# Kernel optimization log

Hardware: AMD Instinct MI355X
Metric: run time of the kernel (lower is better)

The kernel has to match this reference:

```python
import jax, jax.numpy as jnp
import numpy as np

B, S, HID, NH = 2, 2048, 2048, 16
HD = HID // NH          # head_size = 128
ROPE_THETA = 10000.0
SCALING = HD ** -0.5


def setup_inputs() -> dict:
    key = jax.random.key(0)
    ks = jax.random.split(key, 8)
    std = 1.0 / np.sqrt(HID)
    inp = {
        "hidden_states": jax.random.normal(ks[0], (B, S, HID), jnp.float32),
        "positions": jnp.broadcast_to(jnp.arange(S, dtype=jnp.int32), (B, S)),
        "wq": jax.random.normal(ks[1], (HID, HID), jnp.float32) * std,
        "bq": jax.random.normal(ks[2], (HID,), jnp.float32) * 0.02,
        "wk": jax.random.normal(ks[3], (HID, HID), jnp.float32) * std,
        "bk": jax.random.normal(ks[4], (HID,), jnp.float32) * 0.02,
        "wv": jax.random.normal(ks[5], (HID, HID), jnp.float32) * std,
        "bv": jax.random.normal(ks[6], (HID,), jnp.float32) * 0.02,
        "wc": jax.random.normal(ks[7], (HID, HID), jnp.float32) * std,
    }
    return inp


def _rope_neox(x, positions):
    # x: [B, S, NH, HD]; positions: [B, S] int
    half = HD // 2
    inv_freq = 1.0 / (ROPE_THETA ** (jnp.arange(half, dtype=jnp.float32) * (2.0 / HD)))
    freqs = positions.astype(jnp.float32)[..., None] * inv_freq      # [B,S,half]
    cos = jnp.cos(freqs)[:, :, None, :]                               # [B,S,1,half]
    sin = jnp.sin(freqs)[:, :, None, :]
    x1, x2 = x[..., :half], x[..., half:]
    return jnp.concatenate([x1 * cos - x2 * sin, x2 * cos + x1 * sin], axis=-1)


def reference(hidden_states, positions, wq, bq, wk, bk, wv, bv, wc):
    # fused QKV projections
    q = hidden_states @ wq + bq
    k = hidden_states @ wk + bk
    v = hidden_states @ wv + bv
    q = q.reshape(B, S, NH, HD)
    k = k.reshape(B, S, NH, HD)
    v = v.reshape(B, S, NH, HD)
    # neox-style rotary embedding over full head dim
    q = _rope_neox(q, positions)
    k = _rope_neox(k, positions)
    # causal self-attention (prefill path of RadixAttention)
    scores = jnp.einsum("bqhd,bkhd->bhqk", q, k) * SCALING
    causal = jnp.tril(jnp.ones((S, S), dtype=bool))
    scores = jnp.where(causal, scores, jnp.finfo(scores.dtype).min)
    probs = jax.nn.softmax(scores, axis=-1)
    attn = jnp.einsum("bhqk,bkhd->bqhd", probs, v).reshape(B, S, HID)
    # output projection (no bias)
    return attn @ wc
```

## Files before the change

kernel.cpp:

```cpp
#include <hip/hip_runtime.h>
#include <stdint.h>

constexpr int Bsz = 2;
constexpr int Ssz = 2048;
constexpr int Hid = 2048;
constexpr int NHd = 16;
constexpr int Hd  = 128;
constexpr int Mrows = Bsz * Ssz;

typedef __bf16 bf16;
typedef __bf16 bf16x8 __attribute__((ext_vector_type(8)));
typedef __bf16 bf16x4 __attribute__((ext_vector_type(4)));
typedef float  f32x4  __attribute__((ext_vector_type(4)));
typedef float  f32x16 __attribute__((ext_vector_type(16)));

__device__ __forceinline__ void gload_lds16(const bf16* g, bf16* l) {
  __builtin_amdgcn_global_load_lds((const __attribute__((address_space(1))) void*)g,
                                   (__attribute__((address_space(3))) void*)l, 16, 0, 0);
}

__device__ __forceinline__ uint32_t pkbf(bf16 a, bf16 b) {
  union { bf16 hh[2]; uint32_t u; } x;
  x.hh[0] = a; x.hh[1] = b;
  return x.u;
}
__device__ __forceinline__ uint32_t pkff(float a, float b) {
  return pkbf((bf16)a, (bf16)b);
}

__global__ void k_cvt(const float* __restrict__ in, bf16* __restrict__ out, int n4) {
  int i = blockIdx.x * blockDim.x + threadIdx.x;
  if (i >= n4) return;
  float4 v = ((const float4*)in)[i];
  bf16x4 o = { (bf16)v.x, (bf16)v.y, (bf16)v.z, (bf16)v.w };
  ((bf16x4*)out)[i] = o;
}

__global__ void k_wtrans(const float* __restrict__ w0, const float* __restrict__ w1,
                         const float* __restrict__ w2, const float* __restrict__ w3,
                         bf16* __restrict__ out) {
  __shared__ float tile[64][65];
  const int z = blockIdx.z;
  const float* w = (z == 0) ? w0 : (z == 1) ? w1 : (z == 2) ? w2 : w3;
  bf16* o = out + (size_t)z * Hid * Hid;
  const int n0 = blockIdx.x * 64, k0 = blockIdx.y * 64;
  const int tid = threadIdx.x;
  {
    const int row = tid >> 4, col = (tid & 15) * 4;
#pragma unroll
    for (int i = 0; i < 4; i++) {
      float4 v = *(const float4*)&w[(size_t)(k0 + row + i * 16) * Hid + n0 + col];
      tile[row + i * 16][col + 0] = v.x;
      tile[row + i * 16][col + 1] = v.y;
      tile[row + i * 16][col + 2] = v.z;
      tile[row + i * 16][col + 3] = v.w;
    }
  }
  __syncthreads();
  {
    const int n = tid >> 2, ks = (tid & 3) * 16;
    union { bf16x8 v[2]; bf16 e[16]; } pk;
#pragma unroll
    for (int j = 0; j < 16; j++) pk.e[j] = (bf16)tile[ks + j][n];
    bf16* op = &o[(size_t)(n0 + n) * Hid + k0 + ks];
    *(bf16x8*)op = pk.v[0];
    *(bf16x8*)(op + 8) = pk.v[1];
  }
}

__device__ __forceinline__ bf16x8 rdfrag(const bf16* t, int row, int kslot) {
  return *(const bf16x8*)((const char*)t + row * 128 + (((kslot ^ (row & 7)) & 7) << 4));
}

__device__ __forceinline__ void stage_half(const bf16* g, bf16* l, int w, int lane) {
  const int rsub = lane >> 3;
  const int slot = (lane & 7) ^ rsub;
#pragma unroll
  for (int j = 0; j < 2; ++j) {
    const int blk = w * 2 + j;
    gload_lds16(g + (size_t)(blk * 8 + rsub) * Hid + slot * 8, l + blk * 512);
  }
}

__device__ __forceinline__ void stage_192(const bf16* g, bf16* l, int w, int lane) {
  const int rsub = lane >> 3;
  const int slot = (lane & 7) ^ rsub;
#pragma unroll
  for (int j = 0; j < 3; ++j) {
    const int blk = w * 3 + j;
    gload_lds16(g + (size_t)(blk * 8 + rsub) * Hid + slot * 8, l + blk * 512);
  }
}

#define PH_BAR() __builtin_amdgcn_s_barrier()

__global__ __launch_bounds__(512, 1) void k_qkv(const bf16* __restrict__ A,
                                                const bf16* __restrict__ Bt,
                                                const float* __restrict__ biasq,
                                                const float* __restrict__ biask,
                                                const float* __restrict__ biasv,
                                                bf16* __restrict__ Qo, bf16* __restrict__ Ko,
                                                bf16* __restrict__ Vo) {
  constexpr int KK = Hid;
  constexpr int NT = KK / 64;
  __shared__ bf16 smA[2][256 * 64];
  __shared__ bf16 smB[3][192 * 64];
  const int hw = blockIdx.y * gridDim.x + blockIdx.x;
  const int chunk = hw & 7, within = hw >> 3;
  const int cr = chunk & 1, cc = chunk >> 1;
  const int mt = cr * 8 + (within & 7);
  const int nt = cc * 8 + (within >> 3);
  const int m0 = mt * 256, n0 = nt * 192;
  const int tid = threadIdx.x, lane = tid & 63, w = tid >> 6;
  const int wm = w >> 2, wn = w & 3;
  const int frow = lane & 15, a4 = lane >> 4;
  const bf16* Ag = A + (size_t)m0 * KK;
  const bf16* Bg = Bt + (size_t)n0 * KK;
  f32x4 acc[8][3] = {};
  stage_half(Ag,                    smA[0],            w, lane);
  stage_half(Ag + (size_t)128 * KK, smA[0] + 128 * 64, w, lane);
  stage_192 (Bg,                    smB[0],            w, lane);
  stage_192 (Bg + 64,               smB[1],            w, lane);
  asm volatile("s_waitcnt vmcnt(3)" ::: "memory");
  __builtin_amdgcn_sched_barrier(0);
  __builtin_amdgcn_s_barrier();
  for (int kt = 0; kt < NT; ++kt) {
    const bf16* At  = smA[kt & 1];
    const bf16* Btl = smB[kt % 3];
    const bool more1 = (kt + 1) < NT;
    const bool more2 = (kt + 2) < NT;
    bf16x8 afA[4][2], afB[4][2], bfr[3][2];
#pragma unroll
    for (int f = 0; f < 4; ++f)
#pragma unroll
      for (int kk = 0; kk < 2; ++kk)
        afA[f][kk] = rdfrag(At, wm * 128 + f * 16 + frow, kk * 4 + a4);
#pragma unroll
    for (int nf = 0; nf < 3; ++nf)
#pragma unroll
      for (int kk = 0; kk < 2; ++kk)
        bfr[nf][kk] = rdfrag(Btl, wn * 48 + nf * 16 + frow, kk * 4 + a4);
    if (more1) {
      bf16* As2 = smA[(kt + 1) & 1];
      const size_t kn = (size_t)(kt + 1) * 64;
      stage_half(Ag + kn,                    As2,            w, lane);
      stage_half(Ag + (size_t)128 * KK + kn, As2 + 128 * 64, w, lane);
    }
    PH_BAR();
    __builtin_amdgcn_s_setprio(1);
#pragma unroll
    for (int f = 0; f < 4; ++f)
#pragma unroll
      for (int nf = 0; nf < 2; ++nf)
#pragma unroll
        for (int kk = 0; kk < 2; ++kk)
          acc[f][nf] = __builtin_amdgcn_mfma_f32_16x16x32_bf16(
              afA[f][kk], bfr[nf][kk], acc[f][nf], 0, 0, 0);
    __builtin_amdgcn_s_setprio(0);
    __builtin_amdgcn_s_barrier();
#pragma unroll
    for (int f = 0; f < 4; ++f)
#pragma unroll
      for (int kk = 0; kk < 2; ++kk)
        afB[f][kk] = rdfrag(At, wm * 128 + 64 + f * 16 + frow, kk * 4 + a4);
    if (more2) stage_192(Bg + (size_t)(kt + 2) * 64, smB[(kt + 2) % 3], w, lane);
    PH_BAR();
    __builtin_amdgcn_s_setprio(1);
#pragma unroll
    for (int f = 0; f < 4; ++f)
#pragma unroll
      for (int nf = 0; nf < 2; ++nf)
#pragma unroll
        for (int kk = 0; kk < 2; ++kk)
          acc[4 + f][nf] = __builtin_amdgcn_mfma_f32_16x16x32_bf16(
              afB[f][kk], bfr[nf][kk], acc[4 + f][nf], 0, 0, 0);
    __builtin_amdgcn_s_setprio(0);
    __builtin_amdgcn_s_barrier();
    __builtin_amdgcn_s_setprio(1);
#pragma unroll
    for (int f = 0; f < 4; ++f)
#pragma unroll
      for (int kk = 0; kk < 2; ++kk)
        acc[f][2] = __builtin_amdgcn_mfma_f32_16x16x32_bf16(
            afA[f][kk], bfr[2][kk], acc[f][2], 0, 0, 0);
#pragma unroll
    for (int f = 0; f < 4; ++f)
#pragma unroll
      for (int kk = 0; kk < 2; ++kk)
        acc[4 + f][2] = __builtin_amdgcn_mfma_f32_16x16x32_bf16(
            afB[f][kk], bfr[2][kk], acc[4 + f][2], 0, 0, 0);
    __builtin_amdgcn_s_setprio(0);
    if (more1) {
      if (more2) { asm volatile("s_waitcnt vmcnt(3)" ::: "memory"); }
      else       { asm volatile("s_waitcnt vmcnt(0)" ::: "memory"); }
      __builtin_amdgcn_sched_barrier(0);
    }
    __builtin_amdgcn_s_barrier();
  }
#pragma unroll
  for (int nf = 0; nf < 3; ++nf) {
    const int col = n0 + wn * 48 + nf * 16 + frow;
    const int z = col >> 11;
    const float* bias = (z == 0) ? biasq : (z == 1) ? biask : biasv;
    bf16* o = (z == 0) ? Qo : (z == 1) ? Ko : Vo;
    const float oscale = (z == 1) ? (float)(0.08838834764831845 * 1.4426950408889634) : 1.0f;
    const float bb_ = bias[col & 2047];
    const int h = (col >> 7) & 15, hd = col & (Hd - 1);
#pragma unroll
    for (int mf = 0; mf < 8; ++mf) {
#pragma unroll
      for (int r = 0; r < 4; ++r) {
        const int row = m0 + wm * 128 + mf * 16 + a4 * 4 + r;
        const int bb = row >> 11, ss = row & (Ssz - 1);
        o[(((size_t)bb * NHd + h) * Ssz + ss) * Hd + hd] = (bf16)((acc[mf][nf][r] + bb_) * oscale);
      }
    }
  }
}

template <int CHM, int CHN>
__global__ __launch_bounds__(512, 1) void k_gemm(const bf16* __restrict__ A,
                                                 const bf16* __restrict__ Bt,
                                                 float* __restrict__ Fo) {
  constexpr int KK = Hid;
  constexpr int NT = KK / 64;
  __shared__ bf16 smA[2][256 * 64];
  __shared__ bf16 smB[3][128 * 64];
  const int hw = blockIdx.y * gridDim.x + blockIdx.x;
  const int chunk = hw & 7, within = hw >> 3;
  const int chunk_rows = gridDim.y / CHM;
  const int cr = chunk % chunk_rows, cc = chunk / chunk_rows;
  const int mt = cr * CHM + within % CHM;
  const int nt = cc * CHN + within / CHM;
  const int m0 = mt * 256, n0 = nt * 128;
  const int tid = threadIdx.x, lane = tid & 63, w = tid >> 6;
  const int wm = w >> 2, wn = w & 3;
  const int frow = lane & 15, a4 = lane >> 4;
  const bf16* Ag = A + (size_t)m0 * KK;
  const bf16* Bg = Bt + (size_t)n0 * KK;
  f32x4 acc[8][2] = {};
  stage_half(Ag,                    smA[0],            w, lane);
  stage_half(Ag + (size_t)128 * KK, smA[0] + 128 * 64, w, lane);
  stage_half(Bg,                    smB[0],            w, lane);
  stage_half(Bg + 64,               smB[1],            w, lane);
  asm volatile("s_waitcnt vmcnt(2)" ::: "memory");
  __builtin_amdgcn_sched_barrier(0);
  __builtin_amdgcn_s_barrier();
  for (int kt = 0; kt < NT; ++kt) {
    const bf16* At  = smA[kt & 1];
    const bf16* Btl = smB[kt % 3];
    const bool more1 = (kt + 1) < NT;
    const bool more2 = (kt + 2) < NT;
    bf16x8 afA[4][2], afB[4][2], bfr[2][2];
#pragma unroll
    for (int f = 0; f < 4; ++f)
#pragma unroll
      for (int kk = 0; kk < 2; ++kk)
        afA[f][kk] = rdfrag(At, wm * 128 + f * 16 + frow, kk * 4 + a4);
#pragma unroll
    for (int nf = 0; nf < 2; ++nf)
#pragma unroll
      for (int kk = 0; kk < 2; ++kk)
        bfr[nf][kk] = rdfrag(Btl, wn * 32 + nf * 16 + frow, kk * 4 + a4);
    if (more1) {
      bf16* As2 = smA[(kt + 1) & 1];
      const size_t kn = (size_t)(kt + 1) * 64;
      stage_half(Ag + kn,                    As2,            w, lane);
      stage_half(Ag + (size_t)128 * KK + kn, As2 + 128 * 64, w, lane);
    }
    PH_BAR();
    __builtin_amdgcn_s_setprio(1);
#pragma unroll
    for (int f = 0; f < 4; ++f)
#pragma unroll
      for (int nf = 0; nf < 2; ++nf)
#pragma unroll
        for (int kk = 0; kk < 2; ++kk)
          acc[f][nf] = __builtin_amdgcn_mfma_f32_16x16x32_bf16(
              afA[f][kk], bfr[nf][kk], acc[f][nf], 0, 0, 0);
    __builtin_amdgcn_s_setprio(0);
    __builtin_amdgcn_s_barrier();
#pragma unroll
    for (int f = 0; f < 4; ++f)
#pragma unroll
      for (int kk = 0; kk < 2; ++kk)
        afB[f][kk] = rdfrag(At, wm * 128 + 64 + f * 16 + frow, kk * 4 + a4);
    if (more2) stage_half(Bg + (size_t)(kt + 2) * 64, smB[(kt + 2) % 3], w, lane);
    PH_BAR();
    __builtin_amdgcn_s_setprio(1);
#pragma unroll
    for (int f = 0; f < 4; ++f)
#pragma unroll
      for (int nf = 0; nf < 2; ++nf)
#pragma unroll
        for (int kk = 0; kk < 2; ++kk)
          acc[4 + f][nf] = __builtin_amdgcn_mfma_f32_16x16x32_bf16(
              afB[f][kk], bfr[nf][kk], acc[4 + f][nf], 0, 0, 0);
    __builtin_amdgcn_s_setprio(0);
    if (more1) {
      if (more2) { asm volatile("s_waitcnt vmcnt(2)" ::: "memory"); }
      else       { asm volatile("s_waitcnt vmcnt(0)" ::: "memory"); }
      __builtin_amdgcn_sched_barrier(0);
    }
    __builtin_amdgcn_s_barrier();
  }
#pragma unroll
  for (int mf = 0; mf < 8; ++mf)
#pragma unroll
    for (int nf = 0; nf < 2; ++nf) {
      const int col = n0 + wn * 32 + nf * 16 + frow;
#pragma unroll
      for (int r = 0; r < 4; ++r) {
        const int row = m0 + wm * 128 + mf * 16 + a4 * 4 + r;
        Fo[(size_t)row * Hid + col] = acc[mf][nf][r];
      }
    }
}

__global__ void k_rope(bf16* __restrict__ Kk, const int* __restrict__ pos) {
  const int idx = blockIdx.x * 256 + threadIdx.x;
  const int i = idx & 63;
  const int s = (idx >> 6) & (Ssz - 1);
  const int bh = idx >> 17;
  const int b = bh >> 4;
  const float p = (float)pos[b * Ssz + s];
  const float f = p * exp2f(-(float)i * 0.20762050593046014f);
  float sn, cs;
  sincosf(f, &sn, &cs);
  const size_t base = ((size_t)bh * Ssz + s) * Hd;
  float x1 = (float)Kk[base + i], x2 = (float)Kk[base + i + 64];
  Kk[base + i]      = (bf16)(x1 * cs - x2 * sn);
  Kk[base + i + 64] = (bf16)(x2 * cs + x1 * sn);
}

__global__ __launch_bounds__(256, 2) void k_attn(const bf16* __restrict__ Qg,
                                                 const bf16* __restrict__ Kg,
                                                 const bf16* __restrict__ Vg,
                                                 const int* __restrict__ pos,
                                                 bf16* __restrict__ AO) {
  const int bid = blockIdx.x;
  const int slot = bid & 255;
  const int bh = slot & 31;
  const int xch = slot >> 5;
  const int qc = (bid >> 8) ? (15 - xch) : xch;
  const int tid = threadIdx.x, lane = tid & 63, w = tid >> 6;
  const int l31 = lane & 31, h = lane >> 5;
  __shared__ bf16 Ks[2][64 * 128];
  __shared__ bf16 Vt[2][128 * 72];
  const size_t hbase = (size_t)bh * Ssz * Hd;
  const int q0 = qc * 128 + w * 32;
  bf16x8 qf[8];
  {
    const bf16* qp = Qg + hbase + (size_t)(q0 + l31) * Hd + h * 8;
#pragma unroll
    for (int c = 0; c < 8; c++) qf[c] = *(const bf16x8*)(qp + c * 16);
  }
  {
    const float p = (float)pos[(bh >> 4) * Ssz + (q0 + l31)];
#pragma unroll
    for (int c = 0; c < 4; c++) {
#pragma unroll
      for (int j = 0; j < 8; j++) {
        const int i = c * 16 + 8 * h + j;
        const float f = p * exp2f(-(float)i * 0.20762050593046014f);
        float sn, cs;
        sincosf(f, &sn, &cs);
        const float x1 = (float)qf[c][j], x2 = (float)qf[c + 4][j];
        qf[c][j]     = (bf16)(x1 * cs - x2 * sn);
        qf[c + 4][j] = (bf16)(x2 * cs + x1 * sn);
      }
    }
  }
  float m = -1e30f, lsum = 0.f;
  f32x16 o[4] = {};
  const int NT = 2 * (qc + 1);
  const int r4  = (tid >> 4) << 2;
  const int hd0 = (tid & 15) << 3;
  bf16x8 vv[4];
#pragma unroll
  for (int p = 0; p < 4; p++)
    vv[p] = *(const bf16x8*)(Vg + hbase + (size_t)(r4 + p) * Hd + hd0);
  __builtin_amdgcn_sched_barrier(0);
#pragma unroll
  for (int i = 0; i < 4; i++) {
    const int db  = (w * 4 + i) * 1024 + (lane << 4);
    const int row = db >> 8;
    const int cb  = (db & 255) ^ ((row & 7) << 4);
    gload_lds16(Kg + hbase + row * Hd + (cb >> 1), Ks[0] + (w * 4 + i) * 512);
  }
  for (int t = 0; t < NT; ++t) {
    const int kv0 = t * 64;
    const int cur = t & 1;
    asm volatile("s_waitcnt vmcnt(4)" ::: "memory");
#pragma unroll
    for (int j = 0; j < 8; j++) {
      uint2 wv;
      wv.x = pkbf(vv[0][j], vv[1][j]);
      wv.y = pkbf(vv[2][j], vv[3][j]);
      const int hd = hd0 + j;
      const int cb = (r4 * 2) ^ (((hd >> 3) & 7) << 4);
      *(uint2*)((char*)(Vt[cur]) + hd * 144 + cb) = wv;
    }
    const int tn = (t + 1 < NT) ? t + 1 : t;
    const size_t nb = (size_t)tn * 64;
#pragma unroll
    for (int p = 0; p < 4; p++)
      vv[p] = *(const bf16x8*)(Vg + hbase + (nb + r4 + p) * Hd + hd0);
    __builtin_amdgcn_sched_barrier(0);
#pragma unroll
    for (int i = 0; i < 4; i++) {
      const int db  = (w * 4 + i) * 1024 + (lane << 4);
      const int row = db >> 8;
      const int cb  = (db & 255) ^ ((row & 7) << 4);
      gload_lds16(Kg + hbase + (nb + row) * Hd + (cb >> 1), Ks[cur ^ 1] + (w * 4 + i) * 512);
    }
    asm volatile("s_waitcnt vmcnt(8) lgkmcnt(0)" ::: "memory");
    __builtin_amdgcn_sched_barrier(0);
    __builtin_amdgcn_s_barrier();
    if (kv0 <= q0 + 31) {
      const bf16* KsC = Ks[cur];
      const bf16* VtC = Vt[cur];
      f32x16 s0 = {}, s1 = {};
      __builtin_amdgcn_s_setprio(1);
#pragma unroll
      for (int c = 0; c < 8; c++) {
        const int cb = (c * 32 + h * 16) ^ ((l31 & 7) << 4);
        bf16x8 k0 = *(const bf16x8*)((const char*)KsC + l31 * 256 + cb);
        bf16x8 k1 = *(const bf16x8*)((const char*)KsC + (32 + l31) * 256 + cb);
        s0 = __builtin_amdgcn_mfma_f32_32x32x16_bf16(k0, qf[c], s0, 0, 0, 0);
        s1 = __builtin_amdgcn_mfma_f32_32x32x16_bf16(k1, qf[c], s1, 0, 0, 0);
      }
      __builtin_amdgcn_s_setprio(0);
      if (kv0 + 63 > q0) {
        const int qg = q0 + l31;
        const int kb = kv0 + 4 * h;
#pragma unroll
        for (int r = 0; r < 16; r++) {
          const int cr = (r & 3) + 8 * (r >> 2);
          if (kb + cr > qg)      s0[r] = -1e30f;
          if (kb + 32 + cr > qg) s1[r] = -1e30f;
        }
      }
      float tm = s0[0];
#pragma unroll
      for (int r = 1; r < 16; r++) tm = fmaxf(tm, s0[r]);
#pragma unroll
      for (int r = 0; r < 16; r++) tm = fmaxf(tm, s1[r]);
      tm = fmaxf(tm, __shfl_xor(tm, 32));
      if (!__all(tm - m <= 8.0f)) {
        const float mn = fmaxf(m, tm);
        const float rs = exp2f(m - mn);
        m = mn; lsum *= rs;
#pragma unroll
        for (int ct = 0; ct < 4; ct++)
#pragma unroll
          for (int r = 0; r < 16; r++) o[ct][r] *= rs;
      }
      float ps = 0.f;
#pragma unroll
      for (int r = 0; r < 16; r++) { s0[r] = exp2f(s0[r] - m); ps += s0[r]; }
#pragma unroll
      for (int r = 0; r < 16; r++) { s1[r] = exp2f(s1[r] - m); ps += s1[r]; }
      ps += __shfl_xor(ps, 32);
      lsum += ps;
      uint32_t gw[8][2];
#pragma unroll
      for (int g = 0; g < 4; g++) {
        gw[g][0]     = pkff(s0[4 * g], s0[4 * g + 1]);
        gw[g][1]     = pkff(s0[4 * g + 2], s0[4 * g + 3]);
        gw[4 + g][0] = pkff(s1[4 * g], s1[4 * g + 1]);
        gw[4 + g][1] = pkff(s1[4 * g + 2], s1[4 * g + 3]);
      }
#pragma unroll
      for (int kc = 0; kc < 4; kc++) {
        const uint32_t a0 = gw[2 * kc][0], a1 = gw[2 * kc][1];
        const uint32_t b0 = gw[2 * kc + 1][0], b1 = gw[2 * kc + 1][1];
        const uint32_t sd0 = h ? a0 : b0, sd1 = h ? a1 : b1;
        const uint32_t r0 = (uint32_t)__shfl_xor((int)sd0, 32);
        const uint32_t r1 = (uint32_t)__shfl_xor((int)sd1, 32);
        union { uint32_t u[4]; bf16x8 v; } pa;
        pa.u[0] = h ? r0 : a0; pa.u[1] = h ? r1 : a1;
        pa.u[2] = h ? b0 : r0; pa.u[3] = h ? b1 : r1;
        __builtin_amdgcn_s_setprio(1);
#pragma unroll
        for (int ct = 0; ct < 4; ct++) {
          const int row = ct * 32 + l31;
          const int cb = (kc * 32 + h * 16) ^ (((row >> 3) & 7) << 4);
          bf16x8 vf = *(const bf16x8*)((const char*)VtC + row * 144 + cb);
          o[ct] = __builtin_amdgcn_mfma_f32_32x32x16_bf16(pa.v, vf, o[ct], 0, 0, 0);
        }
        __builtin_amdgcn_s_setprio(0);
      }
    }
    __builtin_amdgcn_s_barrier();
  }
  const float linv = 1.0f / lsum;
  float li[16];
#pragma unroll
  for (int r = 0; r < 16; r++)
    li[r] = __shfl(linv, (r & 3) + 8 * (r >> 2) + 4 * h);
  const int b = bh >> 4, hh = bh & 15;
#pragma unroll
  for (int ct = 0; ct < 4; ct++) {
#pragma unroll
    for (int r = 0; r < 16; r++) {
      const int qrow = q0 + (r & 3) + 8 * (r >> 2) + 4 * h;
      AO[((size_t)b * Ssz + qrow) * Hid + hh * Hd + ct * 32 + l31] = (bf16)(o[ct][r] * li[r]);
    }
  }
}

extern "C" void kernel_launch(void* const* d_in, const int* in_sizes, int n_in,
                              void* d_out, int out_size, void* d_ws, size_t ws_size,
                              hipStream_t stream) {
  (void)in_sizes; (void)n_in; (void)out_size; (void)ws_size;
  const float* hidden   = (const float*)d_in[0];
  const int*   positions= (const int*)d_in[1];
  const float* wq = (const float*)d_in[2];
  const float* bq = (const float*)d_in[3];
  const float* wk = (const float*)d_in[4];
  const float* bk = (const float*)d_in[5];
  const float* wv = (const float*)d_in[6];
  const float* bv = (const float*)d_in[7];
  const float* wc = (const float*)d_in[8];
  float* out = (float*)d_out;

  char* ws = (char*)d_ws;
  bf16* WT  = (bf16*)ws;
  bf16* Hbf = (bf16*)(ws + (size_t)4 * Hid * Hid * 2);
  bf16* Qb  = (bf16*)(ws + (size_t)4 * Hid * Hid * 2 + (size_t)Mrows * Hid * 2);
  bf16* Kb  = Qb + (size_t)Mrows * Hid;
  bf16* Vb  = Kb + (size_t)Mrows * Hid;

  k_cvt<<<dim3(Mrows * Hid / 4 / 256), dim3(256), 0, stream>>>(hidden, Hbf, Mrows * Hid / 4);
  k_wtrans<<<dim3(Hid / 64, Hid / 64, 4), dim3(256), 0, stream>>>(wq, wk, wv, wc, WT);
  k_qkv<<<dim3(32, 16), dim3(512), 0, stream>>>(
      Hbf, WT, bq, bk, bv, Qb, Kb, Vb);
  k_rope<<<dim3(Bsz * NHd * Ssz * 64 / 256), dim3(256), 0, stream>>>(Kb, positions);
  k_attn<<<dim3(512), dim3(256), 0, stream>>>(Qb, Kb, Vb, positions, Hbf );
  k_gemm<8, 4><<<dim3(16, 16), dim3(512), 0, stream>>>(
      Hbf, WT + (size_t)3 * Hid * Hid, out);
}
```

Before: 262.0 us.

## Retile QKV GEMM to 256x256 blocks with quarter-tile pipelined staging

The QKV projection kernel moves from 256x192 output tiles with triple-buffered B to 256x256 tiles. A and B are now double-buffered in 128-row halves, and each k-step is split into four MFMA phases, with half-tile global-to-LDS loads interleaved between them. The grid shrinks from 512 to 384 blocks, and each wave now computes a 128x64 sub-tile, which raises arithmetic intensity and cuts redundant A loads. The trade-offs are more accumulator registers, fewer blocks for the CUs (possible tail imbalance), and tighter waitcnt and barrier choreography.

```diff
diff --git a/kernel.cpp b/kernel.cpp
--- a/kernel.cpp
+++ b/kernel.cpp
@@ -82,16 +82,6 @@
   }
 }
 
-__device__ __forceinline__ void stage_192(const bf16* g, bf16* l, int w, int lane) {
-  const int rsub = lane >> 3;
-  const int slot = (lane & 7) ^ rsub;
-#pragma unroll
-  for (int j = 0; j < 3; ++j) {
-    const int blk = w * 3 + j;
-    gload_lds16(g + (size_t)(blk * 8 + rsub) * Hid + slot * 8, l + blk * 512);
-  }
-}
-
 #define PH_BAR() __builtin_amdgcn_s_barrier()
 
 __global__ __launch_bounds__(512, 1) void k_qkv(const bf16* __restrict__ A,
@@ -103,107 +93,141 @@
                                                 bf16* __restrict__ Vo) {
   constexpr int KK = Hid;
   constexpr int NT = KK / 64;
-  __shared__ bf16 smA[2][256 * 64];
-  __shared__ bf16 smB[3][192 * 64];
+  __shared__ bf16 smA[2][2][128 * 64];
+  __shared__ bf16 smB[2][2][128 * 64];
   const int hw = blockIdx.y * gridDim.x + blockIdx.x;
   const int chunk = hw & 7, within = hw >> 3;
-  const int cr = chunk & 1, cc = chunk >> 1;
-  const int mt = cr * 8 + (within & 7);
-  const int nt = cc * 8 + (within >> 3);
-  const int m0 = mt * 256, n0 = nt * 192;
+  const int mt = (chunk & 3) * 4 + (within & 3);
+  const int nt = (chunk >> 2) * 12 + (within >> 2);
+  const int m0 = mt * 256, n0 = nt * 256;
   const int tid = threadIdx.x, lane = tid & 63, w = tid >> 6;
   const int wm = w >> 2, wn = w & 3;
   const int frow = lane & 15, a4 = lane >> 4;
   const bf16* Ag = A + (size_t)m0 * KK;
   const bf16* Bg = Bt + (size_t)n0 * KK;
-  f32x4 acc[8][3] = {};
-  stage_half(Ag,                    smA[0],            w, lane);
-  stage_half(Ag + (size_t)128 * KK, smA[0] + 128 * 64, w, lane);
-  stage_192 (Bg,                    smB[0],            w, lane);
-  stage_192 (Bg + 64,               smB[1],            w, lane);
-  asm volatile("s_waitcnt vmcnt(3)" ::: "memory");
+  const int bbase = (wn & 1) * 64;
+  f32x4 acc[8][4] = {};
+
+#define STG_A(v, half) stage_half(Ag + (size_t)(half) * 128 * KK + (size_t)(v) * 64, \
+                                  smA[(v) & 1][half], w, lane)
+#define STG_B(v, half) stage_half(Bg + (size_t)(half) * 128 * KK + (size_t)(v) * 64, \
+                                  smB[(v) & 1][half], w, lane)
+#define PH_OPEN()                                        \
+  PH_BAR();                                              \
+  asm volatile("s_waitcnt lgkmcnt(0)" ::: "memory");     \
+  __builtin_amdgcn_sched_barrier(0);                     \
+  __builtin_amdgcn_s_setprio(1)
+#define PH_CLOSE() __builtin_amdgcn_s_setprio(0)
+
+  STG_A(0, 0); STG_A(0, 1); STG_B(0, 0); STG_B(0, 1);
+  STG_B(1, 0); STG_B(1, 1);
+  asm volatile("s_waitcnt vmcnt(4)" ::: "memory");
   __builtin_amdgcn_sched_barrier(0);
   __builtin_amdgcn_s_barrier();
-  for (int kt = 0; kt < NT; ++kt) {
-    const bf16* At  = smA[kt & 1];
-    const bf16* Btl = smB[kt % 3];
-    const bool more1 = (kt + 1) < NT;
-    const bool more2 = (kt + 2) < NT;
-    bf16x8 afA[4][2], afB[4][2], bfr[3][2];
-#pragma unroll
-    for (int f = 0; f < 4; ++f)
-#pragma unroll
-      for (int kk = 0; kk < 2; ++kk)
-        afA[f][kk] = rdfrag(At, wm * 128 + f * 16 + frow, kk * 4 + a4);
-#pragma unroll
-    for (int nf = 0; nf < 3; ++nf)
-#pragma unroll
-      for (int kk = 0; kk < 2; ++kk)
-        bfr[nf][kk] = rdfrag(Btl, wn * 48 + nf * 16 + frow, kk * 4 + a4);
-    if (more1) {
-      bf16* As2 = smA[(kt + 1) & 1];
-      const size_t kn = (size_t)(kt + 1) * 64;
-      stage_half(Ag + kn,                    As2,            w, lane);
-      stage_half(Ag + (size_t)128 * KK + kn, As2 + 128 * 64, w, lane);
-    }
-    PH_BAR();
-    __builtin_amdgcn_s_setprio(1);
-#pragma unroll
-    for (int f = 0; f < 4; ++f)
-#pragma unroll
-      for (int nf = 0; nf < 2; ++nf)
+
+  for (int t = 0; t < NT / 2; ++t) {
+    const int u = 2 * t;
+    const bool more = (u + 2) < NT;
+    bf16x8 afL[4][2], afH[4][2], bfL[2][2], bfH[2][2];
+#pragma unroll 1
+    for (int half = 0; half < 2; ++half) {
+      const int kt = u + half;
+      const bf16* Ah = smA[kt & 1][wm];
+      const bf16* Bh = smB[kt & 1][wn >> 1];
+#pragma unroll
+      for (int f = 0; f < 4; ++f)
 #pragma unroll
         for (int kk = 0; kk < 2; ++kk)
-          acc[f][nf] = __builtin_amdgcn_mfma_f32_16x16x32_bf16(
-              afA[f][kk], bfr[nf][kk], acc[f][nf], 0, 0, 0);
-    __builtin_amdgcn_s_setprio(0);
-    __builtin_amdgcn_s_barrier();
-#pragma unroll
-    for (int f = 0; f < 4; ++f)
-#pragma unroll
-      for (int kk = 0; kk < 2; ++kk)
-        afB[f][kk] = rdfrag(At, wm * 128 + 64 + f * 16 + frow, kk * 4 + a4);
-    if (more2) stage_192(Bg + (size_t)(kt + 2) * 64, smB[(kt + 2) % 3], w, lane);
-    PH_BAR();
-    __builtin_amdgcn_s_setprio(1);
-#pragma unroll
-    for (int f = 0; f < 4; ++f)
-#pragma unroll
-      for (int nf = 0; nf < 2; ++nf)
+          afL[f][kk] = rdfrag(Ah, f * 16 + frow, kk * 4 + a4);
+#pragma unroll
+      for (int f = 0; f < 2; ++f)
 #pragma unroll
         for (int kk = 0; kk < 2; ++kk)
-          acc[4 + f][nf] = __builtin_amdgcn_mfma_f32_16x16x32_bf16(
-              afB[f][kk], bfr[nf][kk], acc[4 + f][nf], 0, 0, 0);
-    __builtin_amdgcn_s_setprio(0);
-    __builtin_amdgcn_s_barrier();
-    __builtin_amdgcn_s_setprio(1);
-#pragma unroll
-    for (int f = 0; f < 4; ++f)
-#pragma unroll
-      for (int kk = 0; kk < 2; ++kk)
-        acc[f][2] = __builtin_amdgcn_mfma_f32_16x16x32_bf16(
-            afA[f][kk], bfr[2][kk], acc[f][2], 0, 0, 0);
-#pragma unroll
-    for (int f = 0; f < 4; ++f)
-#pragma unroll
-      for (int kk = 0; kk < 2; ++kk)
-        acc[4 + f][2] = __builtin_amdgcn_mfma_f32_16x16x32_bf16(
-            afB[f][kk], bfr[2][kk], acc[4 + f][2], 0, 0, 0);
-    __builtin_amdgcn_s_setprio(0);
-    if (more1) {
-      if (more2) { asm volatile("s_waitcnt vmcnt(3)" ::: "memory"); }
-      else       { asm volatile("s_waitcnt vmcnt(0)" ::: "memory"); }
-      __builtin_amdgcn_sched_barrier(0);
-    }
-    __builtin_amdgcn_s_barrier();
-  }
-#pragma unroll
-  for (int nf = 0; nf < 3; ++nf) {
-    const int col = n0 + wn * 48 + nf * 16 + frow;
-    const int z = col >> 11;
-    const float* bias = (z == 0) ? biasq : (z == 1) ? biask : biasv;
-    bf16* o = (z == 0) ? Qo : (z == 1) ? Ko : Vo;
-    const float oscale = (z == 1) ? (float)(0.08838834764831845 * 1.4426950408889634) : 1.0f;
+          bfL[f][kk] = rdfrag(Bh, bbase + f * 16 + frow, kk * 4 + a4);
+      if (half == 0)            STG_A(u + 1, 0);
+      else if (more)            STG_A(u + 2, 0);
+      asm volatile("s_waitcnt lgkmcnt(8)" ::: "memory");
+      PH_OPEN();
+#pragma unroll
+      for (int f = 0; f < 4; ++f)
+#pragma unroll
+        for (int n = 0; n < 2; ++n)
+#pragma unroll
+          for (int kk = 0; kk < 2; ++kk)
+            acc[f][n] = __builtin_amdgcn_mfma_f32_16x16x32_bf16(
+                afL[f][kk], bfL[n][kk], acc[f][n], 0, 0, 0);
+      PH_CLOSE();
+      PH_BAR();
+#pragma unroll
+      for (int f = 0; f < 2; ++f)
+#pragma unroll
+        for (int kk = 0; kk < 2; ++kk)
+          bfH[f][kk] = rdfrag(Bh, bbase + 32 + f * 16 + frow, kk * 4 + a4);
+      if (half == 0)            STG_A(u + 1, 1);
+      else if (more)            STG_A(u + 2, 1);
+      PH_OPEN();
+#pragma unroll
+      for (int f = 0; f < 4; ++f)
+#pragma unroll
+        for (int n = 0; n < 2; ++n)
+#pragma unroll
+          for (int kk = 0; kk < 2; ++kk)
+            acc[f][2 + n] = __builtin_amdgcn_mfma_f32_16x16x32_bf16(
+                afL[f][kk], bfH[n][kk], acc[f][2 + n], 0, 0, 0);
+      PH_CLOSE();
+      PH_BAR();
+#pragma unroll
+      for (int f = 0; f < 4; ++f)
+#pragma unroll
+        for (int kk = 0; kk < 2; ++kk)
+          afH[f][kk] = rdfrag(Ah, 64 + f * 16 + frow, kk * 4 + a4);
+      if (more) { if (half == 0) STG_B(u + 2, 0);
+                  else           STG_B(u + 3, 0); }
+      PH_OPEN();
+#pragma unroll
+      for (int f = 0; f < 4; ++f)
+#pragma unroll
+        for (int n = 0; n < 2; ++n)
+#pragma unroll
+          for (int kk = 0; kk < 2; ++kk)
+            acc[4 + f][n] = __builtin_amdgcn_mfma_f32_16x16x32_bf16(
+                afH[f][kk], bfL[n][kk], acc[4 + f][n], 0, 0, 0);
+      PH_CLOSE();
+      PH_BAR();
+      if (more) { if (half == 0) STG_B(u + 2, 1);
+                  else           STG_B(u + 3, 1); }
+      PH_OPEN();
+#pragma unroll
+      for (int f = 0; f < 4; ++f)
+#pragma unroll
+        for (int n = 0; n < 2; ++n)
+#pragma unroll
+          for (int kk = 0; kk < 2; ++kk)
+            acc[4 + f][2 + n] = __builtin_amdgcn_mfma_f32_16x16x32_bf16(
+                afH[f][kk], bfH[n][kk], acc[4 + f][2 + n], 0, 0, 0);
+      PH_CLOSE();
+      if (half == 0) {
+        if (more) { asm volatile("s_waitcnt vmcnt(4)" ::: "memory"); }
+        else      { asm volatile("s_waitcnt vmcnt(0)" ::: "memory"); }
+        __builtin_amdgcn_sched_barrier(0);
+      } else if (more) {
+        asm volatile("s_waitcnt vmcnt(4)" ::: "memory");
+        __builtin_amdgcn_sched_barrier(0);
+      }
+      PH_BAR();
+    }
+  }
+#undef STG_A
+#undef STG_B
+#undef PH_OPEN
+#undef PH_CLOSE
+  const int z = n0 >> 11;
+  const float* bias = (z == 0) ? biasq : (z == 1) ? biask : biasv;
+  bf16* o = (z == 0) ? Qo : (z == 1) ? Ko : Vo;
+  const float oscale = (z == 1) ? (float)(0.08838834764831845 * 1.4426950408889634) : 1.0f;
+#pragma unroll
+  for (int nf = 0; nf < 4; ++nf) {
+    const int col = n0 + wn * 64 + nf * 16 + frow;
     const float bb_ = bias[col & 2047];
     const int h = (col >> 7) & 15, hd = col & (Hd - 1);
 #pragma unroll
@@ -534,7 +558,7 @@
 
   k_cvt<<<dim3(Mrows * Hid / 4 / 256), dim3(256), 0, stream>>>(hidden, Hbf, Mrows * Hid / 4);
   k_wtrans<<<dim3(Hid / 64, Hid / 64, 4), dim3(256), 0, stream>>>(wq, wk, wv, wc, WT);
-  k_qkv<<<dim3(32, 16), dim3(512), 0, stream>>>(
+  k_qkv<<<dim3(24, 16), dim3(512), 0, stream>>>(
       Hbf, WT, bq, bk, bv, Qb, Kb, Vb);
   k_rope<<<dim3(Bsz * NHd * Ssz * 64 / 256), dim3(256), 0, stream>>>(Kb, positions);
   k_attn<<<dim3(512), dim3(256), 0, stream>>>(Qb, Kb, Vb, positions, Hbf );
```

After: 289.3 us. 1.1x slower.
